# Performance work log

Measured on AMD Instinct MI355X. Metric: run time of the kernel, lower is better.

Reference implementation:

```python
import jax, jax.numpy as jnp
import numpy as np

GAMMA = 0.5          # cfg.distribution_loss.triplet_loss_gamma
POS_RADIUS = 0.6     # cfg.fine_loss.positive_radius
BIG = 1e12

B, K = 4096, 64      # node correspondences, knn points per node
N = K + 1            # matching_scores has one slack row/col


def setup_inputs() -> dict:
    key = jax.random.key(0)
    k1, k2, k3, k4, k5 = jax.random.split(key, 5)
    pos_pts = jax.random.normal(k1, (B, K, 3), dtype=jnp.float32)
    # anchor points near positives so some pairs fall inside positive_radius
    anc_pts = pos_pts + 0.3 * jax.random.normal(k2, (B, K, 3), dtype=jnp.float32)
    pos_masks = jax.random.uniform(k3, (B, K)) < 0.9
    anc_masks = jax.random.uniform(k4, (B, K)) < 0.9
    matching_scores = jax.random.normal(k5, (B, N, N), dtype=jnp.float32)
    transform = jnp.eye(4, dtype=jnp.float32)  # rigid SE(3); identity keeps pos/neg masks realistic
    return {
        'pos_node_corr_knn_points': pos_pts,
        'anc_node_corr_knn_points': anc_pts,
        'pos_node_corr_knn_masks': pos_masks,
        'anc_node_corr_knn_masks': anc_masks,
        'matching_scores': matching_scores,
        'transform': transform,
    }


def _apply_transform(points, transform):
    R = transform[:3, :3]
    t = transform[:3, 3]
    return jnp.einsum('bkd,ed->bke', points, R) + t


def _pairwise_sq_dist(x, y):
    # (b,n,3),(b,m,3) -> (b,n,m) squared distances
    x2 = jnp.sum(x * x, axis=-1)
    y2 = jnp.sum(y * y, axis=-1)
    xy = jnp.einsum('bnd,bmd->bnm', x, y)
    return x2[:, :, None] - 2.0 * xy + y2[:, None, :]


def reference(pos_node_corr_knn_points, anc_node_corr_knn_points,
              pos_node_corr_knn_masks, anc_node_corr_knn_masks,
              matching_scores, transform):
    b, n, m = matching_scores.shape
    anc = _apply_transform(anc_node_corr_knn_points, transform)
    dists = _pairwise_sq_dist(pos_node_corr_knn_points, anc)  # (b, n-1, m-1)

    gt_masks = pos_node_corr_knn_masks[:, :, None] & anc_node_corr_knn_masks[:, None, :]
    gt_corr = (dists < POS_RADIUS ** 2) & gt_masks
    gt_neg = dists > (2.0 * POS_RADIUS) ** 2
    row_none = jnp.sum(gt_corr, axis=2) == 0   # (b, n-1): rows w/o correspondence -> slack col
    col_none = jnp.sum(gt_corr, axis=1) == 0   # (b, m-1): cols w/o correspondence -> slack row

    pos_mask = (jnp.zeros((b, n, m), dtype=bool)
                .at[:, :-1, :-1].set(gt_corr)
                .at[:, :-1, -1].set(row_none)
                .at[:, -1, :-1].set(col_none))
    neg_mask = (jnp.zeros((b, n, m), dtype=bool)
                .at[:, :-1, :-1].set(gt_neg)
                .at[:, :-1, -1].set(~row_none)
                .at[:, -1, :-1].set(~col_none))

    ms = matching_scores

    # ---- row direction (over pos knn rows, all m cols) ----
    pm = pos_mask[:, :-1, :]
    nm = neg_mask[:, :-1, :]
    ms_r = ms[:, :-1, :]
    pos_score = jnp.sum(jnp.where(pm, -ms_r, 0.0), axis=2) / jnp.sum(pm, axis=2)  # (b, n-1); count>=1
    neg_score = jnp.where(nm, -ms_r, BIG)                                          # (b, n-1, m)
    gap1 = pos_score[:, :, None] - neg_score
    per1 = jnp.log(jnp.sum(jnp.maximum(gap1 + GAMMA, 0.0), axis=2) + 1.0)          # (b, n-1)
    keep1 = pos_score != BIG
    loss1 = jnp.sum(jnp.where(keep1, per1, 0.0)) / jnp.maximum(jnp.sum(keep1), 1)

    # ---- column direction (over anc knn cols, all n rows) ----
    pmc = pos_mask[:, :, :-1]
    nmc = neg_mask[:, :, :-1]
    ms_c = ms[:, :, :-1]
    pos_score_inv = jnp.sum(jnp.where(pmc, -ms_c, 0.0), axis=1) / jnp.sum(pmc, axis=1)  # (b, m-1)
    neg_score_inv = jnp.where(nmc, -ms_c, BIG)                                           # (b, n, m-1)
    gap2 = jnp.transpose(pos_score_inv[:, None, :] - neg_score_inv, (0, 2, 1))           # (b, m-1, n)
    per2 = jnp.log(jnp.sum(jnp.maximum(gap2 + GAMMA, 0.0), axis=2) + 1.0)                # (b, m-1)
    keep2 = pos_score_inv != BIG
    loss2 = jnp.sum(jnp.where(keep2, per2, 0.0)) / jnp.maximum(jnp.sum(keep2), 1)

    return (loss1 + loss2) / 2.0
```

## Files before the change

### kernel.cpp

```cpp
#include <hip/hip_runtime.h>
#include <hip/hip_fp16.h>


#define R2_POS 0.36f
#define R2_NEG 1.44f
#define GAMMA_C 0.5f
#define NBATCH 4096
#define NPART (NBATCH * 2)
#define HCNEG -1024.0f

typedef _Float16 hf2 __attribute__((ext_vector_type(2)));
typedef float f4v __attribute__((ext_vector_type(4)));

__device__ __forceinline__ int maskbit(const void* p, int i, int mode) {
    if (mode == 0) return ((const unsigned*)p)[i] != 0u;
    if (mode == 1) return ((const unsigned short*)p)[i] != 0;
    return ((const unsigned char*)p)[i] != 0;
}

__device__ __forceinline__ float sload(float v) {
    return __uint_as_float(__builtin_amdgcn_readfirstlane(__float_as_uint(v)));
}

__device__ __forceinline__ float rlane(float v, int i) {
    return __uint_as_float(__builtin_amdgcn_readlane(__float_as_uint(v), i));
}

__global__ __launch_bounds__(128, 3)
void fused_kernel(const float* __restrict__ posp,
                  const float* __restrict__ ancp,
                  const void* __restrict__ pmp,
                  const void* __restrict__ amp,
                  const float* __restrict__ msp,
                  const float* __restrict__ xfp,
                  float* __restrict__ partials) {
    const int tid = threadIdx.x;
    const int b = blockIdx.x;
    const int w = tid >> 6;
    const int l = tid & 63;

    unsigned mw0 = ((const unsigned*)pmp)[l];
    bool okw = (mw0 == 0u) || (mw0 == 1u) || (mw0 == 0x3F800000u);
    unsigned hh0 = mw0 & 0xFFFFu, hh1 = mw0 >> 16;
    bool okh = (hh0 == 0u || hh0 == 0x3F80u) && (hh1 == 0u || hh1 == 0x3F80u);
    int mmode = (__ballot(okw) == ~0ULL) ? 0 : ((__ballot(okh) == ~0ULL) ? 1 : 2);

    float T[12];
#pragma unroll
    for (int e = 0; e < 3; ++e)
#pragma unroll
        for (int d = 0; d < 4; ++d) T[e * 4 + d] = sload(xfp[e * 4 + d]);

    const int pb = (b * 64 + l) * 3;
    const float px = posp[pb], py = posp[pb + 1], pz = posp[pb + 2];
    const float r0 = ancp[pb], r1 = ancp[pb + 1], r2 = ancp[pb + 2];
    const float ax = T[0] * r0 + T[1] * r1 + T[2]  * r2 + T[3];
    const float ay = T[4] * r0 + T[5] * r1 + T[6]  * r2 + T[7];
    const float az = T[8] * r0 + T[9] * r1 + T[10] * r2 + T[11];

    const int mi = b * 64 + l;
    const unsigned long long pmM = __ballot(maskbit(pmp, mi, mmode) != 0);
    const unsigned long long amM = __ballot(maskbit(amp, mi, mmode) != 0);

    float psum = 0.f; int pcnt = 0; float slack;
    hf2 hc[32];

    if (w == 0) {
        const float* rowp = msp + (size_t)b * 4225 + l * 65;
        f4v ch[16];
#pragma unroll
        for (int c = 0; c < 16; ++c)
            __builtin_memcpy(&ch[c], rowp + 4 * c, 16);
        slack = rowp[64];
#pragma unroll
        for (int c = 0; c < 16; ++c) asm volatile("" : "+v"(ch[c]));
        asm volatile("" : "+v"(slack));
        asm volatile("" ::: "memory");

        const bool pmL = (pmM >> l) & 1ULL;
#pragma unroll
        for (int jj = 0; jj < 32; ++jj) {
            float h0, h1;
#pragma unroll
            for (int s = 0; s < 2; ++s) {
                const int j = 2 * jj + s;
                float v = ch[j >> 2][j & 3];
                float bx = rlane(ax, j);
                float by = rlane(ay, j);
                float bz = rlane(az, j);
                float dx = px - bx, dy = py - by, dz = pz - bz;
                float d2 = dx * dx + dy * dy + dz * dz;
                bool pos = pmL && ((amM >> j) & 1ULL) && (d2 < R2_POS);
                psum -= pos ? v : 0.f;
                pcnt += pos ? 1 : 0;
                float hcv = (d2 > R2_NEG) ? v : HCNEG;
                if (s == 0) h0 = hcv; else h1 = hcv;
            }
            hf2 h; h[0] = (_Float16)h0; h[1] = (_Float16)h1;
            hc[jj] = h;
        }
    } else {
        const float* mcol = msp + (size_t)b * 4225 + l;
        float vcol[64];
#pragma unroll
        for (int r = 0; r < 64; ++r) vcol[r] = mcol[r * 65];
        slack = mcol[64 * 65];
#pragma unroll
        for (int r = 0; r < 64; ++r) asm volatile("" : "+v"(vcol[r]));
        asm volatile("" : "+v"(slack));
        asm volatile("" ::: "memory");

        const bool amL = (amM >> l) & 1ULL;
#pragma unroll
        for (int jj = 0; jj < 32; ++jj) {
            float h0, h1;
#pragma unroll
            for (int s = 0; s < 2; ++s) {
                const int r = 2 * jj + s;
                float v = vcol[r];
                float qx = rlane(px, r);
                float qy = rlane(py, r);
                float qz = rlane(pz, r);
                float dx = qx - ax, dy = qy - ay, dz = qz - az;
                float d2 = dx * dx + dy * dy + dz * dz;
                bool pos = ((pmM >> r) & 1ULL) && amL && (d2 < R2_POS);
                psum -= pos ? v : 0.f;
                pcnt += pos ? 1 : 0;
                float hcv = (d2 > R2_NEG) ? v : HCNEG;
                if (s == 0) h0 = hcv; else h1 = hcv;
            }
            hf2 h; h[0] = (_Float16)h0; h[1] = (_Float16)h1;
            hc[jj] = h;
        }
    }

    const float ps = pcnt ? psum / (float)pcnt : -slack;

    const _Float16 ch16 = (_Float16)(ps + GAMMA_C);
    const hf2 C2 = {ch16, ch16};
    const hf2 Z = {(_Float16)0.f, (_Float16)0.f};
    float hv = 0.f;
#if __has_builtin(__builtin_amdgcn_fdot2)
    const hf2 ONE2 = {(_Float16)1.f, (_Float16)1.f};
#pragma unroll
    for (int k = 0; k < 32; ++k) {
        hf2 x = hc[k] + C2;
        x = __builtin_elementwise_max(x, Z);
        hv = __builtin_amdgcn_fdot2(x, ONE2, hv, false);
    }
#else
#pragma unroll
    for (int k = 0; k < 32; ++k) {
        hf2 x = hc[k] + C2;
        x = __builtin_elementwise_max(x, Z);
        hv += (float)x[0] + (float)x[1];
    }
#endif
    if (pcnt) hv += fmaxf(ps + slack + GAMMA_C, 0.f);
    float result = __logf(hv + 1.f);

#pragma unroll
    for (int off = 1; off < 64; off <<= 1)
        result += __shfl_xor(result, off, 64);
    if (l == 0) partials[b * 2 + w] = result;
}

__global__ void finalize_kernel(const float* __restrict__ partials,
                                unsigned* __restrict__ out) {
    __shared__ float red[4];
    const int tid = threadIdx.x;
    float s = 0.f;
    for (int i = tid; i < NPART; i += 256) s += partials[i];
#pragma unroll
    for (int off = 1; off < 64; off <<= 1) s += __shfl_xor(s, off, 64);
    if ((tid & 63) == 0) red[tid >> 6] = s;
    __syncthreads();
    if (tid == 0) {
        float tot = red[0] + red[1] + red[2] + red[3];
        float loss = tot * (1.0f / (2.0f * NBATCH * 64.0f));
        unsigned bits = __float_as_uint(loss);
        unsigned h = (bits + 0x7FFFu + ((bits >> 16) & 1u)) >> 16;
        out[0] = (h << 16) | h;
    }
}

extern "C" void kernel_launch(void* const* d_in, const int* in_sizes, int n_in,
                              void* d_out, int out_size, void* d_ws, size_t ws_size,
                              hipStream_t stream) {
    (void)in_sizes; (void)n_in; (void)out_size; (void)ws_size;
    const float* posp = (const float*)d_in[0];
    const float* ancp = (const float*)d_in[1];
    const void* pmp = d_in[2];
    const void* amp = d_in[3];
    const float* msp = (const float*)d_in[4];
    const float* xfp = (const float*)d_in[5];

    fused_kernel<<<NBATCH, 128, 0, stream>>>(posp, ancp, pmp, amp, msp, xfp,
                                             (float*)d_ws);
    finalize_kernel<<<1, 256, 0, stream>>>((const float*)d_ws,
                                           (unsigned*)d_out);
}
```

Measured before the change: 129.1 us.

## Split each row/column pass across two waves with LDS partial-sum exchange

Each block now uses four waves instead of two. Each direction (row and column) is split between two waves that each handle half of the 64 entries. Partial positive sums and counts are exchanged through shared memory, and hinge sums are combined by one wave before the log and reduction. The aim is to halve per-thread register arrays and serial work so more waves are resident to hide memory latency, at the cost of two block barriers and some duplicated setup loads.

```diff
diff --git a/kernel.cpp b/kernel.cpp
--- a/kernel.cpp
+++ b/kernel.cpp
@@ -26,7 +26,7 @@
     return __uint_as_float(__builtin_amdgcn_readlane(__float_as_uint(v), i));
 }
 
-__global__ __launch_bounds__(128, 3)
+__global__ __launch_bounds__(256, 4)
 void fused_kernel(const float* __restrict__ posp,
                   const float* __restrict__ ancp,
                   const void* __restrict__ pmp,
@@ -34,10 +34,15 @@
                   const float* __restrict__ msp,
                   const float* __restrict__ xfp,
                   float* __restrict__ partials) {
+    __shared__ float2 xps[256];
+    __shared__ float  xhv[128];
+
     const int tid = threadIdx.x;
     const int b = blockIdx.x;
-    const int w = tid >> 6;
+    const int wv = tid >> 6;
     const int l = tid & 63;
+    const int role = wv >> 1;
+    const int W = wv & 1;
 
     unsigned mw0 = ((const unsigned*)pmp)[l];
     bool okw = (mw0 == 0u) || (mw0 == 1u) || (mw0 == 0x3F800000u);
@@ -62,29 +67,30 @@
     const unsigned long long pmM = __ballot(maskbit(pmp, mi, mmode) != 0);
     const unsigned long long amM = __ballot(maskbit(amp, mi, mmode) != 0);
 
-    float psum = 0.f; int pcnt = 0; float slack;
-    hf2 hc[32];
-
-    if (w == 0) {
+    float psum = 0.f, pcnt = 0.f, slack;
+    hf2 hc[16];
+
+    if (role == 0) {
         const float* rowp = msp + (size_t)b * 4225 + l * 65;
-        f4v ch[16];
-#pragma unroll
-        for (int c = 0; c < 16; ++c)
-            __builtin_memcpy(&ch[c], rowp + 4 * c, 16);
+        f4v ch[8];
+#pragma unroll
+        for (int c = 0; c < 8; ++c)
+            __builtin_memcpy(&ch[c], rowp + 32 * W + 4 * c, 16);
         slack = rowp[64];
 #pragma unroll
-        for (int c = 0; c < 16; ++c) asm volatile("" : "+v"(ch[c]));
+        for (int c = 0; c < 8; ++c) asm volatile("" : "+v"(ch[c]));
         asm volatile("" : "+v"(slack));
         asm volatile("" ::: "memory");
 
         const bool pmL = (pmM >> l) & 1ULL;
 #pragma unroll
-        for (int jj = 0; jj < 32; ++jj) {
+        for (int jj = 0; jj < 16; ++jj) {
             float h0, h1;
 #pragma unroll
             for (int s = 0; s < 2; ++s) {
-                const int j = 2 * jj + s;
-                float v = ch[j >> 2][j & 3];
+                const int q = 2 * jj + s;
+                const int j = 32 * W + q;
+                float v = ch[q >> 2][q & 3];
                 float bx = rlane(ax, j);
                 float by = rlane(ay, j);
                 float bz = rlane(az, j);
@@ -92,7 +98,7 @@
                 float d2 = dx * dx + dy * dy + dz * dz;
                 bool pos = pmL && ((amM >> j) & 1ULL) && (d2 < R2_POS);
                 psum -= pos ? v : 0.f;
-                pcnt += pos ? 1 : 0;
+                pcnt += pos ? 1.f : 0.f;
                 float hcv = (d2 > R2_NEG) ? v : HCNEG;
                 if (s == 0) h0 = hcv; else h1 = hcv;
             }
@@ -101,23 +107,24 @@
         }
     } else {
         const float* mcol = msp + (size_t)b * 4225 + l;
-        float vcol[64];
-#pragma unroll
-        for (int r = 0; r < 64; ++r) vcol[r] = mcol[r * 65];
+        float vc[32];
+#pragma unroll
+        for (int s = 0; s < 32; ++s) vc[s] = mcol[(32 * W + s) * 65];
         slack = mcol[64 * 65];
 #pragma unroll
-        for (int r = 0; r < 64; ++r) asm volatile("" : "+v"(vcol[r]));
+        for (int s = 0; s < 32; ++s) asm volatile("" : "+v"(vc[s]));
         asm volatile("" : "+v"(slack));
         asm volatile("" ::: "memory");
 
         const bool amL = (amM >> l) & 1ULL;
 #pragma unroll
-        for (int jj = 0; jj < 32; ++jj) {
+        for (int jj = 0; jj < 16; ++jj) {
             float h0, h1;
 #pragma unroll
             for (int s = 0; s < 2; ++s) {
-                const int r = 2 * jj + s;
-                float v = vcol[r];
+                const int q = 2 * jj + s;
+                const int r = 32 * W + q;
+                float v = vc[q];
                 float qx = rlane(px, r);
                 float qy = rlane(py, r);
                 float qz = rlane(pz, r);
@@ -125,7 +132,7 @@
                 float d2 = dx * dx + dy * dy + dz * dz;
                 bool pos = ((pmM >> r) & 1ULL) && amL && (d2 < R2_POS);
                 psum -= pos ? v : 0.f;
-                pcnt += pos ? 1 : 0;
+                pcnt += pos ? 1.f : 0.f;
                 float hcv = (d2 > R2_NEG) ? v : HCNEG;
                 if (s == 0) h0 = hcv; else h1 = hcv;
             }
@@ -134,7 +141,13 @@
         }
     }
 
-    const float ps = pcnt ? psum / (float)pcnt : -slack;
+    xps[tid] = make_float2(psum, pcnt);
+    __syncthreads();
+    {
+        float2 o = xps[(wv ^ 1) * 64 + l];
+        psum += o.x; pcnt += o.y;
+    }
+    const float ps = (pcnt != 0.f) ? psum / pcnt : -slack;
 
     const _Float16 ch16 = (_Float16)(ps + GAMMA_C);
     const hf2 C2 = {ch16, ch16};
@@ -143,26 +156,31 @@
 #if __has_builtin(__builtin_amdgcn_fdot2)
     const hf2 ONE2 = {(_Float16)1.f, (_Float16)1.f};
 #pragma unroll
-    for (int k = 0; k < 32; ++k) {
+    for (int k = 0; k < 16; ++k) {
         hf2 x = hc[k] + C2;
         x = __builtin_elementwise_max(x, Z);
         hv = __builtin_amdgcn_fdot2(x, ONE2, hv, false);
     }
 #else
 #pragma unroll
-    for (int k = 0; k < 32; ++k) {
+    for (int k = 0; k < 16; ++k) {
         hf2 x = hc[k] + C2;
         x = __builtin_elementwise_max(x, Z);
         hv += (float)x[0] + (float)x[1];
     }
 #endif
-    if (pcnt) hv += fmaxf(ps + slack + GAMMA_C, 0.f);
-    float result = __logf(hv + 1.f);
-
-#pragma unroll
-    for (int off = 1; off < 64; off <<= 1)
-        result += __shfl_xor(result, off, 64);
-    if (l == 0) partials[b * 2 + w] = result;
+
+    if (W) xhv[role * 64 + l] = hv;
+    __syncthreads();
+    if (!W) {
+        float hv_t = hv + xhv[role * 64 + l];
+        if (pcnt != 0.f) hv_t += fmaxf(ps + slack + GAMMA_C, 0.f);
+        float result = __logf(hv_t + 1.f);
+#pragma unroll
+        for (int off = 1; off < 64; off <<= 1)
+            result += __shfl_xor(result, off, 64);
+        if (l == 0) partials[b * 2 + role] = result;
+    }
 }
 
 __global__ void finalize_kernel(const float* __restrict__ partials,
@@ -195,7 +213,7 @@
     const float* msp = (const float*)d_in[4];
     const float* xfp = (const float*)d_in[5];
 
-    fused_kernel<<<NBATCH, 128, 0, stream>>>(posp, ancp, pmp, amp, msp, xfp,
+    fused_kernel<<<NBATCH, 256, 0, stream>>>(posp, ancp, pmp, amp, msp, xfp,
                                              (float*)d_ws);
     finalize_kernel<<<1, 256, 0, stream>>>((const float*)d_ws,
                                            (unsigned*)d_out);
```

Measured after the change: 134.8 us. 4.4% more time.
